# Optimization experiments

Measured on AMD Instinct MI355X. Metric: run time of the kernel, lower is better.

The kernel has to match this reference:

```python
import jax, jax.numpy as jnp
from jax import lax
import numpy as np

B, C, H, W = 32, 32, 64, 64
HD = 128          # hidden_dim per direction
OUT = 128         # output_dim
IN_DIM = 2 * HD + C   # linear input: [x, h_up, h_left]


def setup_inputs() -> dict:
    key = jax.random.key(0)
    ks = jax.random.split(key, 10)
    x = jax.random.normal(ks[0], (B, C, H, W), dtype=jnp.float32)
    # 4 directional MDLSTM cells, params stacked on leading dim
    lin_scale = 1.0 / np.sqrt(IN_DIM)
    W_lin = jax.random.normal(ks[1], (4, 5 * HD, IN_DIM), dtype=jnp.float32) * lin_scale
    b_lin = jax.random.normal(ks[2], (4, 5 * HD), dtype=jnp.float32) * lin_scale
    # peephole weights: torch uses uniform_(0,1); scale down for numeric stability
    Wci = jax.random.uniform(ks[3], (4, 1, HD), dtype=jnp.float32) * 0.1
    Wf1 = jax.random.uniform(ks[4], (4, 1, HD), dtype=jnp.float32) * 0.1
    Wf2 = jax.random.uniform(ks[5], (4, 1, HD), dtype=jnp.float32) * 0.1
    Wco = jax.random.uniform(ks[6], (4, 1, HD), dtype=jnp.float32) * 0.1
    # 1x1 conv: weight [OUT, 4*HD]
    W_conv = jax.random.normal(ks[7], (OUT, 4 * HD), dtype=jnp.float32) / np.sqrt(4 * HD)
    b_conv = jax.random.normal(ks[8], (OUT,), dtype=jnp.float32) * 0.01
    return {"x": x, "W_lin": W_lin, "b_lin": b_lin, "Wci": Wci, "Wf1": Wf1,
            "Wf2": Wf2, "Wco": Wco, "W_conv": W_conv, "b_conv": b_conv}


def _mdlstm_scan(x, Wl, bl, wci, wf1, wf2, wco):
    # x: [H, W, B, C] -> h: [H, W, B, HD].
    # Recurrence: (i,j) depends on (i-1,j) (up) and (i,j-1) (left), zero at borders
    # (clamped-index reads in the torch code hit still-zero h/c entries).
    Wdim, Bb = x.shape[1], x.shape[2]
    zeros = jnp.zeros((Bb, HD), x.dtype)

    def col_step(carry, inp):
        h_left, c_left = carry
        x_ij, h_up, c_up = inp                       # [B,C], [B,HD], [B,HD]
        z = jnp.concatenate([x_ij, h_up, h_left], axis=1) @ Wl.T + bl  # [B,5HD]
        i_g, f1, f2, g, o = jnp.split(z, 5, axis=1)
        i_g = jax.nn.sigmoid(i_g + wci * c_up + wci * c_left)
        f1 = jax.nn.sigmoid(f1 + wf1 * c_up)
        f2 = jax.nn.sigmoid(f2 + wf2 * c_left)
        c_next = f1 * c_up + f2 * c_left + i_g * jnp.tanh(g)
        o = jax.nn.sigmoid(o + wco * c_next)
        h_next = o * jnp.tanh(c_next)
        return (h_next, c_next), (h_next, c_next)

    def row_step(carry, x_row):
        h_up_row, c_up_row = carry                   # [W, B, HD]
        _, (h_row, c_row) = lax.scan(col_step, (zeros, zeros),
                                     (x_row, h_up_row, c_up_row))
        return (h_row, c_row), h_row

    row_init = (jnp.zeros((Wdim, Bb, HD), x.dtype),
                jnp.zeros((Wdim, Bb, HD), x.dtype))
    _, h_all = lax.scan(row_step, row_init, x)       # [H, W, B, HD]
    return h_all


# direction flips, matching torch order: hf_vf, hr_vf (flip H), hf_vr (flip W), hr_vr
_FLIPS = [(False, False), (True, False), (False, True), (True, True)]


def reference(x, W_lin, b_lin, Wci, Wf1, Wf2, Wco, W_conv, b_conv):
    xp = jnp.transpose(x, (2, 3, 0, 1))              # [H, W, B, C]
    outs = []
    for d, (f0, f1) in enumerate(_FLIPS):
        xi = xp
        if f0:
            xi = xi[::-1]
        if f1:
            xi = xi[:, ::-1]
        # NOTE: original code does NOT flip outputs back before concatenating.
        outs.append(_mdlstm_scan(xi, W_lin[d], b_lin[d], Wci[d], Wf1[d], Wf2[d], Wco[d]))
    comb = jnp.concatenate(outs, axis=3)             # [H, W, B, 4*HD]
    out = jnp.einsum('hwbc,oc->bohw', comb, W_conv) + b_conv[None, :, None, None]
    return out                                       # [B, OUT, H, W]
```

## Files before the change

### kernel.cpp

```cpp
#include <hip/hip_runtime.h>
#include <hip/hip_bf16.h>


#define HDIM 128
#define ZDIM 640
#define KDIM 288

typedef __attribute__((ext_vector_type(2))) float f32x2;

__device__ __forceinline__ float sigmoidf_(float v) {
    return 1.0f / (1.0f + __expf(-v));
}
__device__ __forceinline__ float tanhf_(float v) {
    return 1.0f - 2.0f / (__expf(2.0f * v) + 1.0f);
}

__global__ void prep_weights(const float* __restrict__ W_lin,
                             const float* __restrict__ W_conv,
                             float* __restrict__ Wt, float* __restrict__ Wct) {
    int idx = blockIdx.x * 256 + threadIdx.x;
    const int NLIN = 4 * ZDIM * KDIM;
    if (idx < NLIN) {
        int d = idx / (ZDIM * KDIM);
        int r = idx % (ZDIM * KDIM);
        int n = r / KDIM;
        int k = r % KDIM;
        Wt[d * (ZDIM * KDIM) + k * ZDIM + n] = W_lin[idx];
    } else {
        int idx2 = idx - NLIN;
        if (idx2 < 128 * 512) {
            int o = idx2 / 512, c = idx2 % 512;
            Wct[c * 128 + o] = W_conv[idx2];
        }
    }
}

__global__ __launch_bounds__(256) void transpose_x(const float* __restrict__ x,
                                                   float* __restrict__ x_t) {
    __shared__ float tile[64][65];
    int tb = blockIdx.x >> 6;
    int tj = blockIdx.x & 63;
    int t = threadIdx.x;
    for (int f = t; f < 4096; f += 256) {
        int r = f >> 6, cix = f & 63;
        tile[r][cix] = x[(size_t)(tb * 64 + r) * 4096 + tj * 64 + cix];
    }
    __syncthreads();
    for (int f = t; f < 4096; f += 256) {
        int rr = f >> 6, cc = f & 63;
        x_t[(size_t)(tj * 64 + rr) * 1024 + tb * 64 + cc] = tile[cc][rr];
    }
}

__global__ void fill_sentinel(float* __restrict__ out) {
    out[blockIdx.x * 256 + threadIdx.x] = 1.0e6f;
}

__global__ __launch_bounds__(256) void fused_step(
    const float* __restrict__ x_t,
    const float* __restrict__ Wt,
    const float* __restrict__ b_lin,
    const float* __restrict__ Wci, const float* __restrict__ Wf1,
    const float* __restrict__ Wf2, const float* __restrict__ Wco,
    const float* __restrict__ Wct,
    const float* __restrict__ b_conv,
    float* __restrict__ h_par,
    float* __restrict__ c_par,
    float* __restrict__ out,
    int s, int i0, int nc, int i0p, int ncp, int nstep) {
    __shared__ __align__(16) float smem[32 * KDIM];

    const int t = threadIdx.x;
    const int blk = blockIdx.x;
    const int par = s & 1, parR = par ^ 1;

    if (blk < nstep) {
        int r0 = blk;
        const int cbt = r0 & 1;
        r0 >>= 1;
        const int ci = r0 % nc;
        const int d = r0 / nc;
        const int i = i0 + ci, j = s - i;
        const int fi = (d & 1) ? 63 - i : i;
        const int fj = (d & 2) ? 63 - j : j;
        const int ijf = fi * 64 + fj;

        const size_t slotR = (size_t)(parR * 4 + d) * 64;
        const size_t slotW = (size_t)(par * 4 + d) * 64;

        {
            int row = t >> 3, q = t & 7;
            *(float4*)&smem[row * KDIM + q * 4] =
                *(const float4*)(x_t + (size_t)ijf * 1024 + row * 32 + q * 4);
        }
        {
            const float* hu =
                (i > 0) ? h_par + (slotR + (size_t)(i - 1)) * 4096 : nullptr;
            for (int f = t; f < 1024; f += 256) {
                int row = f >> 5, q = f & 31;
                float4 v = make_float4(0.f, 0.f, 0.f, 0.f);
                if (hu) v = *(const float4*)(hu + row * 128 + q * 4);
                *(float4*)&smem[row * KDIM + 32 + q * 4] = v;
            }
        }
        {
            const float* hl =
                (j > 0) ? h_par + (slotR + (size_t)i) * 4096 : nullptr;
            for (int f = t; f < 1024; f += 256) {
                int row = f >> 5, q = f & 31;
                float4 v = make_float4(0.f, 0.f, 0.f, 0.f);
                if (hl) v = *(const float4*)(hl + row * 128 + q * 4);
                *(float4*)&smem[row * KDIM + 160 + q * 4] = v;
            }
        }
        __syncthreads();

        const int rg = t >> 5;
        const int c2 = t & 31;
        const int cb0 = cbt * 64 + c2 * 2;
        const float* wdp = Wt + (size_t)d * (KDIM * ZDIM) + cb0;
        const float* xrow = smem + (rg * 4) * KDIM;

        f32x2 acc[4][5];
#pragma unroll
        for (int g = 0; g < 5; ++g) {
            f32x2 bv = *(const f32x2*)(b_lin + d * ZDIM + g * 128 + cb0);
#pragma unroll
            for (int rr = 0; rr < 4; ++rr) acc[rr][g] = bv;
        }

#pragma unroll 4
        for (int k = 0; k < KDIM; ++k) {
            const float* wk = wdp + (size_t)k * ZDIM;
            f32x2 wv[5];
#pragma unroll
            for (int g = 0; g < 5; ++g) wv[g] = *(const f32x2*)(wk + g * 128);
#pragma unroll
            for (int rr = 0; rr < 4; ++rr) {
                float xs = xrow[rr * KDIM + k];
                f32x2 xv = {xs, xs};
#pragma unroll
                for (int g = 0; g < 5; ++g)
                    acc[rr][g] += xv * wv[g];
            }
        }

        const size_t ru = (slotR + (size_t)(i - 1)) * 4096;
        const size_t rl = (slotR + (size_t)i) * 4096;
        const size_t wb = (slotW + (size_t)i) * 4096;
#pragma unroll
        for (int cc = 0; cc < 2; ++cc) {
            const int col = cb0 + cc;
            const float wciv = Wci[d * HDIM + col];
            const float wf1v = Wf1[d * HDIM + col];
            const float wf2v = Wf2[d * HDIM + col];
            const float wcov = Wco[d * HDIM + col];
#pragma unroll
            for (int rr = 0; rr < 4; ++rr) {
                const int b = rg * 4 + rr;
                float cu = (i > 0) ? c_par[ru + b * 128 + col] : 0.f;
                float cl = (j > 0) ? c_par[rl + b * 128 + col] : 0.f;
                float ig = sigmoidf_(acc[rr][0][cc] + wciv * (cu + cl));
                float f1 = sigmoidf_(acc[rr][1][cc] + wf1v * cu);
                float f2 = sigmoidf_(acc[rr][2][cc] + wf2v * cl);
                float cn = f1 * cu + f2 * cl + ig * tanhf_(acc[rr][3][cc]);
                float oo = sigmoidf_(acc[rr][4][cc] + wcov * cn);
                float hn = oo * tanhf_(cn);
                c_par[wb + b * 128 + col] = cn;
                h_par[wb + b * 128 + col] = hn;
            }
        }
    } else {
        int cb2 = blk - nstep;
        int btc = cb2 & 3, cip = cb2 >> 2;
        int ip = i0p + cip, jp = (s - 1) - ip;
        float* hs = smem;

        for (int f = t; f < 1024; f += 256) {
            int dd = f >> 8, rem = f & 255;
            int bb = rem >> 5, k4 = rem & 31;
            float4 v = *(const float4*)(
                h_par + ((size_t)(parR * 4 + dd) * 64 + ip) * 4096 +
                (btc * 8 + bb) * 128 + k4 * 4);
            *(float4*)&hs[bb * 512 + dd * 128 + k4 * 4] = v;
        }
        __syncthreads();

        const int o = t & 127, half = t >> 7;
        float acc[4];
#pragma unroll
        for (int q = 0; q < 4; ++q) acc[q] = b_conv[o];
#pragma unroll 4
        for (int c = 0; c < 512; ++c) {
            float wv = Wct[c * 128 + o];
#pragma unroll
            for (int q = 0; q < 4; ++q)
                acc[q] = fmaf(hs[(half * 4 + q) * 512 + c], wv, acc[q]);
        }
#pragma unroll
        for (int q = 0; q < 4; ++q) {
            int b = btc * 8 + half * 4 + q;
            out[(size_t)(b * 128 + o) * 4096 + ip * 64 + jp] = acc[q];
        }
    }
}

extern "C" void kernel_launch(void* const* d_in, const int* in_sizes, int n_in,
                              void* d_out, int out_size, void* d_ws,
                              size_t ws_size, hipStream_t stream) {
    const float* x = (const float*)d_in[0];
    const float* W_lin = (const float*)d_in[1];
    const float* b_lin = (const float*)d_in[2];
    const float* Wci = (const float*)d_in[3];
    const float* Wf1 = (const float*)d_in[4];
    const float* Wf2 = (const float*)d_in[5];
    const float* Wco = (const float*)d_in[6];
    const float* W_conv = (const float*)d_in[7];
    const float* b_conv = (const float*)d_in[8];
    float* out = (float*)d_out;

    const size_t N_PAR = 2ull * 4 * 64 * 32 * 128;
    const size_t N_WT = 4ull * KDIM * ZDIM;
    const size_t N_WCT = 512ull * 128;
    const size_t N_XT = 4096ull * 1024;
    float* h_par = (float*)d_ws;
    float* c_par = h_par + N_PAR;
    float* Wt = c_par + N_PAR;
    float* Wct = Wt + N_WT;
    float* x_t = Wct + N_WCT;
    size_t need = (2 * N_PAR + N_WT + N_WCT + N_XT) * 4ull;
    if (ws_size < need) {
        fill_sentinel<<<(out_size + 255) / 256, 256, 0, stream>>>(out);
        return;
    }

    prep_weights<<<3136, 256, 0, stream>>>(W_lin, W_conv, Wt, Wct);
    transpose_x<<<1024, 256, 0, stream>>>(x, x_t);

    for (int s = 0; s <= 127; ++s) {
        int i0 = 0, nc = 0;
        if (s <= 126) {
            i0 = s > 63 ? s - 63 : 0;
            int i1 = s < 63 ? s : 63;
            nc = i1 - i0 + 1;
        }
        int i0p = 0, ncp = 0;
        if (s >= 1) {
            int sp = s - 1;
            i0p = sp > 63 ? sp - 63 : 0;
            int i1p = sp < 63 ? sp : 63;
            ncp = i1p - i0p + 1;
        }
        int nstep = (s <= 126) ? 8 * nc : 0;
        int nconv = 4 * ncp;
        fused_step<<<nstep + nconv, 256, 0, stream>>>(
            x_t, Wt, b_lin, Wci, Wf1, Wf2, Wco, Wct, b_conv, h_par, c_par, out,
            s, i0, nc, i0p, ncp, nstep);
    }
}
```

Measured before the change: 9.498 ms.

## Split step GEMM across twice as many blocks with k-pair interleaved weights

Re-lays out the transposed LSTM weights so consecutive k values are interleaved in pairs, which allows float4 weight loads that cover two k steps. Each block now handles 32 gate columns instead of 64, and each thread 2 batch rows instead of 4, doubling the number of step blocks per diagonal. It also pads the shared-memory row stride and sets an occupancy hint in launch bounds. The aim is more parallelism on small diagonals and fewer load instructions, at the cost of less weight reuse per thread, since each weight now feeds only two rows.

Result: faster. 8.929 ms (-6.0%).

```diff
diff --git a/kernel.cpp b/kernel.cpp
--- a/kernel.cpp
+++ b/kernel.cpp
@@ -5,6 +5,8 @@
 #define HDIM 128
 #define ZDIM 640
 #define KDIM 288
+#define K2DIM 144
+#define ASTR 292
 
 typedef __attribute__((ext_vector_type(2))) float f32x2;
 
@@ -17,7 +19,7 @@
 
 __global__ void prep_weights(const float* __restrict__ W_lin,
                              const float* __restrict__ W_conv,
-                             float* __restrict__ Wt, float* __restrict__ Wct) {
+                             float* __restrict__ Wt2, float* __restrict__ Wct) {
     int idx = blockIdx.x * 256 + threadIdx.x;
     const int NLIN = 4 * ZDIM * KDIM;
     if (idx < NLIN) {
@@ -25,7 +27,7 @@
         int r = idx % (ZDIM * KDIM);
         int n = r / KDIM;
         int k = r % KDIM;
-        Wt[d * (ZDIM * KDIM) + k * ZDIM + n] = W_lin[idx];
+        Wt2[((d * K2DIM + (k >> 1)) * ZDIM + n) * 2 + (k & 1)] = W_lin[idx];
     } else {
         int idx2 = idx - NLIN;
         if (idx2 < 128 * 512) {
@@ -56,9 +58,9 @@
     out[blockIdx.x * 256 + threadIdx.x] = 1.0e6f;
 }
 
-__global__ __launch_bounds__(256) void fused_step(
+__global__ __launch_bounds__(256, 4) void fused_step(
     const float* __restrict__ x_t,
-    const float* __restrict__ Wt,
+    const float* __restrict__ Wt2,
     const float* __restrict__ b_lin,
     const float* __restrict__ Wci, const float* __restrict__ Wf1,
     const float* __restrict__ Wf2, const float* __restrict__ Wco,
@@ -68,16 +70,15 @@
     float* __restrict__ c_par,
     float* __restrict__ out,
     int s, int i0, int nc, int i0p, int ncp, int nstep) {
-    __shared__ __align__(16) float smem[32 * KDIM];
+    __shared__ __align__(16) float smem[32 * ASTR];
 
     const int t = threadIdx.x;
     const int blk = blockIdx.x;
     const int par = s & 1, parR = par ^ 1;
 
     if (blk < nstep) {
-        int r0 = blk;
-        const int cbt = r0 & 1;
-        r0 >>= 1;
+        const int cbt = blk & 3;
+        int r0 = blk >> 2;
         const int ci = r0 % nc;
         const int d = r0 / nc;
         const int i = i0 + ci, j = s - i;
@@ -90,7 +91,7 @@
 
         {
             int row = t >> 3, q = t & 7;
-            *(float4*)&smem[row * KDIM + q * 4] =
+            *(float4*)&smem[row * ASTR + q * 4] =
                 *(const float4*)(x_t + (size_t)ijf * 1024 + row * 32 + q * 4);
         }
         {
@@ -100,7 +101,7 @@
                 int row = f >> 5, q = f & 31;
                 float4 v = make_float4(0.f, 0.f, 0.f, 0.f);
                 if (hu) v = *(const float4*)(hu + row * 128 + q * 4);
-                *(float4*)&smem[row * KDIM + 32 + q * 4] = v;
+                *(float4*)&smem[row * ASTR + 32 + q * 4] = v;
             }
         }
         {
@@ -110,38 +111,42 @@
                 int row = f >> 5, q = f & 31;
                 float4 v = make_float4(0.f, 0.f, 0.f, 0.f);
                 if (hl) v = *(const float4*)(hl + row * 128 + q * 4);
-                *(float4*)&smem[row * KDIM + 160 + q * 4] = v;
+                *(float4*)&smem[row * ASTR + 160 + q * 4] = v;
             }
         }
         __syncthreads();
 
-        const int rg = t >> 5;
-        const int c2 = t & 31;
-        const int cb0 = cbt * 64 + c2 * 2;
-        const float* wdp = Wt + (size_t)d * (KDIM * ZDIM) + cb0;
-        const float* xrow = smem + (rg * 4) * KDIM;
-
-        f32x2 acc[4][5];
+        const int c2 = t & 15, tr = t >> 4;
+        const int cb0 = cbt * 32 + c2 * 2;
+        const float* wbase = Wt2 + (size_t)(d * K2DIM) * 1280 + cb0 * 2;
+        const float* xr0 = smem + (2 * tr) * ASTR;
+        const float* xr1 = xr0 + ASTR;
+
+        f32x2 acc[2][5];
 #pragma unroll
         for (int g = 0; g < 5; ++g) {
             f32x2 bv = *(const f32x2*)(b_lin + d * ZDIM + g * 128 + cb0);
-#pragma unroll
-            for (int rr = 0; rr < 4; ++rr) acc[rr][g] = bv;
+            acc[0][g] = bv;
+            acc[1][g] = bv;
         }
 
 #pragma unroll 4
-        for (int k = 0; k < KDIM; ++k) {
-            const float* wk = wdp + (size_t)k * ZDIM;
-            f32x2 wv[5];
-#pragma unroll
-            for (int g = 0; g < 5; ++g) wv[g] = *(const f32x2*)(wk + g * 128);
-#pragma unroll
-            for (int rr = 0; rr < 4; ++rr) {
-                float xs = xrow[rr * KDIM + k];
-                f32x2 xv = {xs, xs};
-#pragma unroll
-                for (int g = 0; g < 5; ++g)
-                    acc[rr][g] += xv * wv[g];
+        for (int k2 = 0; k2 < K2DIM; ++k2) {
+            const float* wk = wbase + (size_t)k2 * 1280;
+            float4 wv[5];
+#pragma unroll
+            for (int g = 0; g < 5; ++g)
+                wv[g] = *(const float4*)(wk + g * 256);
+            f32x2 a0 = *(const f32x2*)(xr0 + k2 * 2);
+            f32x2 a1 = *(const f32x2*)(xr1 + k2 * 2);
+#pragma unroll
+            for (int g = 0; g < 5; ++g) {
+                f32x2 we = {wv[g].x, wv[g].z};
+                f32x2 wo = {wv[g].y, wv[g].w};
+                acc[0][g] += f32x2{a0.x, a0.x} * we;
+                acc[0][g] += f32x2{a0.y, a0.y} * wo;
+                acc[1][g] += f32x2{a1.x, a1.x} * we;
+                acc[1][g] += f32x2{a1.y, a1.y} * wo;
             }
         }
 
@@ -156,8 +161,8 @@
             const float wf2v = Wf2[d * HDIM + col];
             const float wcov = Wco[d * HDIM + col];
 #pragma unroll
-            for (int rr = 0; rr < 4; ++rr) {
-                const int b = rg * 4 + rr;
+            for (int rr = 0; rr < 2; ++rr) {
+                const int b = 2 * tr + rr;
                 float cu = (i > 0) ? c_par[ru + b * 128 + col] : 0.f;
                 float cl = (j > 0) ? c_par[rl + b * 128 + col] : 0.f;
                 float ig = sigmoidf_(acc[rr][0][cc] + wciv * (cu + cl));
@@ -225,8 +230,8 @@
     const size_t N_XT = 4096ull * 1024;
     float* h_par = (float*)d_ws;
     float* c_par = h_par + N_PAR;
-    float* Wt = c_par + N_PAR;
-    float* Wct = Wt + N_WT;
+    float* Wt2 = c_par + N_PAR;
+    float* Wct = Wt2 + N_WT;
     float* x_t = Wct + N_WCT;
     size_t need = (2 * N_PAR + N_WT + N_WCT + N_XT) * 4ull;
     if (ws_size < need) {
@@ -234,7 +239,7 @@
         return;
     }
 
-    prep_weights<<<3136, 256, 0, stream>>>(W_lin, W_conv, Wt, Wct);
+    prep_weights<<<3136, 256, 0, stream>>>(W_lin, W_conv, Wt2, Wct);
     transpose_x<<<1024, 256, 0, stream>>>(x, x_t);
 
     for (int s = 0; s <= 127; ++s) {
@@ -251,10 +256,10 @@
             int i1p = sp < 63 ? sp : 63;
             ncp = i1p - i0p + 1;
         }
-        int nstep = (s <= 126) ? 8 * nc : 0;
+        int nstep = (s <= 126) ? 16 * nc : 0;
         int nconv = 4 * ncp;
         fused_step<<<nstep + nconv, 256, 0, stream>>>(
-            x_t, Wt, b_lin, Wci, Wf1, Wf2, Wco, Wct, b_conv, h_par, c_par, out,
-            s, i0, nc, i0p, ncp, nstep);
-    }
-}
+            x_t, Wt2, b_lin, Wci, Wf1, Wf2, Wco, Wct, b_conv, h_par, c_par,
+            out, s, i0, nc, i0p, ncp, nstep);
+    }
+}
```
